# Kernel optimization log

Measured on AMD Instinct MI355X. Metric: run time of the kernel, lower is better.

The kernel has to match this reference:

```python
import jax, jax.numpy as jnp
import numpy as np


def setup_inputs() -> dict:
    key = jax.random.key(0)
    ks = jax.random.split(key, 7)
    B, Q, K, H, D, R = 2, 2048, 2048, 16, 64, 32
    queries = jax.random.normal(ks[0], (B, Q, H, D), dtype=jnp.float32)
    keys = jax.random.normal(ks[1], (B, K, H, D), dtype=jnp.float32)
    values = jax.random.normal(ks[2], (B, K, H, D), dtype=jnp.float32)
    att_mask = jax.random.randint(ks[3], (B, Q, K), 0, 2, dtype=jnp.int32)
    relative_att_ids = jax.random.randint(ks[4], (B, Q, K), 0, R, dtype=jnp.int32)
    # TruncatedNormal(stddev=0.5) approximated by clipped normal
    relative_emb_table = jnp.clip(
        0.5 * jax.random.normal(ks[5], (R, H, D), dtype=jnp.float32), -1.0, 1.0)
    relative_bias_table = jnp.zeros((R, H), dtype=jnp.float32)
    return {
        'queries': queries,
        'keys': keys,
        'values': values,
        'att_mask': att_mask,
        'relative_att_ids': relative_att_ids,
        'relative_emb_table': relative_emb_table,
        'relative_bias_table': relative_bias_table,
    }


def reference(queries, keys, values, att_mask, relative_att_ids,
              relative_emb_table, relative_bias_table):
    # content scores: [B,Q,K,H]
    content = jnp.einsum('bqhd,bkhd->bqkh', queries, keys)
    # relative scores per vocab id: [B,Q,R,H]
    all_rel = jnp.einsum('bqhd,rhd->bqrh', queries, relative_emb_table)
    all_rel = all_rel + relative_bias_table  # broadcast [R,H]
    # gather along vocab axis per (q,k): [B,Q,K,H]
    rel = jnp.take_along_axis(
        all_rel, relative_att_ids[:, :, :, None].astype(jnp.int32), axis=2)
    scores = content + rel
    d = queries.shape[-1]
    scores = scores / jnp.sqrt(jnp.asarray(d, scores.dtype))
    mask_adder = -10000.0 * (1.0 - att_mask[:, :, :, None].astype(scores.dtype))
    scores = scores + mask_adder
    probs = jax.nn.softmax(scores, axis=-2)  # softmax over key axis
    return jnp.einsum('bqkh,bkhd->bqhd', probs, values)
```

## Files before the change

kernel.cpp:

```cpp
#include <hip/hip_runtime.h>
#include <hip/hip_fp16.h>
#include <stdint.h>

#define Bn 2
#define Qn 2048
#define Kn 2048
#define Hn 16
#define Dn 64
#define Rn 32

#define LOG2E_8 0.18033688011112042f
#define MASK_NEG -14426.950408889634f

typedef __attribute__((ext_vector_type(8))) short short8v;
typedef __attribute__((ext_vector_type(4))) float f32x4;
typedef __attribute__((ext_vector_type(4))) uint32_t u32x4;

static __device__ __forceinline__ uint16_t bf16rn(float f) {
  uint32_t u = __builtin_bit_cast(uint32_t, f);
  u += 0x7FFFu + ((u >> 16) & 1u);
  return (uint16_t)(u >> 16);
}
static __device__ __forceinline__ float bf16f(uint16_t h) {
  uint32_t u = ((uint32_t)h) << 16;
  return __builtin_bit_cast(float, u);
}
static __device__ __forceinline__ float exp2a(float x) {
  float r; asm("v_exp_f32 %0, %1" : "=v"(r) : "v"(x)); return r;
}
static __device__ __forceinline__ uint32_t cvtpk(float lo, float hi) {
  uint32_t r; asm("v_cvt_pk_bf16_f32 %0, %1, %2" : "=v"(r) : "v"(lo), "v"(hi)); return r;
}
static __device__ __forceinline__ void gl_lds16(const void* g, void* l) {
  __builtin_amdgcn_global_load_lds((const __attribute__((address_space(1))) void*)g,
                                   (__attribute__((address_space(3))) void*)l, 16, 0, 0);
}

__global__ void pack_kernel(const int* __restrict__ ids,
                            const int* __restrict__ msk,
                            uint32_t* __restrict__ outp, int n4) {
  int i = blockIdx.x * 256 + threadIdx.x;
  if (i >= n4) return;
  int4 a = reinterpret_cast<const int4*>(ids)[i];
  int4 m = reinterpret_cast<const int4*>(msk)[i];
  uint32_t v = (uint32_t)((a.x | (m.x << 5)) & 0x3f)
             | ((uint32_t)((a.y | (m.y << 5)) & 0x3f) << 8)
             | ((uint32_t)((a.z | (m.z << 5)) & 0x3f) << 16)
             | ((uint32_t)((a.w | (m.w << 5)) & 0x3f) << 24);
  outp[i] = v;
}

__global__ __launch_bounds__(256) void kfrag6_kernel(const float* __restrict__ Kg,
                                                     const float* __restrict__ Vg,
                                                     uint8_t* __restrict__ frag) {
  const int bid = blockIdx.x;
  const int c = bid & 63;
  const int h = (bid >> 6) & 15;
  const int b = bid >> 10;
  uint8_t* panel = frag + (size_t)(b * 16 + h) * 524288u + (size_t)c * 8192u;
  uint4* kf = reinterpret_cast<uint4*>(panel);
  uint4* vf = reinterpret_cast<uint4*>(panel + 4096);
  const int tid = threadIdx.x;
  const int sdq = tid & 7, srow = (tid >> 3) & 15, stile = tid >> 7;
  const int sg = sdq & 3, sdm = sdq >> 2;
  const float* kp = Kg + ((((size_t)b * Kn) + c * 32 + stile * 16 + srow) * Hn + h) * Dn + (sdm * 32 + sg * 4);
  const float4 x0 = *reinterpret_cast<const float4*>(kp);
  const float4 x1 = *reinterpret_cast<const float4*>(kp + 16);
  const float xs0[4] = {x0.x * LOG2E_8, x0.y * LOG2E_8, x0.z * LOG2E_8, x0.w * LOG2E_8};
  const float xs1[4] = {x1.x * LOG2E_8, x1.y * LOG2E_8, x1.z * LOG2E_8, x1.w * LOG2E_8};
  uint4 uh;
  uh.x = bf16rn(xs0[0]) | ((uint32_t)bf16rn(xs0[1]) << 16);
  uh.y = bf16rn(xs0[2]) | ((uint32_t)bf16rn(xs0[3]) << 16);
  uh.z = bf16rn(xs1[0]) | ((uint32_t)bf16rn(xs1[1]) << 16);
  uh.w = bf16rn(xs1[2]) | ((uint32_t)bf16rn(xs1[3]) << 16);
  kf[(stile * 2 + sdm) * 64 + (srow + 16 * sg)] = uh;
  const int vd = tid & 63, vkq = tid >> 6;
  const float* vp = Vg + ((((size_t)b * Kn) + c * 32 + vkq * 4) * Hn + h) * Dn + vd;
  float v0[4], v1[4];
#pragma unroll
  for (int i = 0; i < 4; ++i) {
    v0[i] = vp[i * (Hn * Dn)];
    v1[i] = vp[(16 + i) * (Hn * Dn)];
  }
  uint4 uv;
  uv.x = bf16rn(v0[0]) | ((uint32_t)bf16rn(v0[1]) << 16);
  uv.y = bf16rn(v0[2]) | ((uint32_t)bf16rn(v0[3]) << 16);
  uv.z = bf16rn(v1[0]) | ((uint32_t)bf16rn(v1[1]) << 16);
  uv.w = bf16rn(v1[2]) | ((uint32_t)bf16rn(v1[3]) << 16);
  vf[(vd >> 4) * 64 + (vd & 15) + 16 * vkq] = uv;
}

__global__ __launch_bounds__(256, 2) void attn7_kernel(
    const float* __restrict__ Qg, const float* __restrict__ Eg,
    const float* __restrict__ biasg, const uint8_t* __restrict__ packed,
    const uint8_t* __restrict__ kfragp, float* __restrict__ outg) {
  __shared__ alignas(16) char smem[75520];
  __half* const tab   = reinterpret_cast<__half*>(smem);
  char* const cb0 = smem + 16896;
  char* const cb1 = smem + 33280;
  float* const q_lds  = reinterpret_cast<float*>(smem + 49664);
  float* const et_lds = reinterpret_cast<float*>(smem + 67072);

  const int tid = threadIdx.x;
  const int lane = tid & 63;
  const int w = tid >> 6;
  const int qr = lane & 15;
  const int g = lane >> 4;

  const int wi = (blockIdx.x & 7) * 64 + (blockIdx.x >> 3);
  const int qt = wi & 15;
  const int h = (wi >> 4) & 15;
  const int b = wi >> 8;
  const int q0 = qt * 128;

  const uint8_t* sbase = kfragp + (size_t)(b * 16 + h) * 524288u +
                         (size_t)w * 4096 + (size_t)lane * 16;
  {
    char* ld = cb0 + w * 4096;
    gl_lds16(sbase, ld);
    gl_lds16(sbase + 1024, ld + 1024);
    gl_lds16(sbase + 2048, ld + 2048);
    gl_lds16(sbase + 3072, ld + 3072);
  }

  short8v qhi[2][2];

#pragma unroll
  for (int half = 0; half < 2; ++half) {
    {
      const int row = tid >> 2, dq = (tid & 3) * 16;
      const float4* s4 = reinterpret_cast<const float4*>(
          Qg + (((size_t)b * Qn + q0 + half * 64 + row) * Hn + h) * Dn + dq);
      float4* dst = reinterpret_cast<float4*>(&q_lds[row * 68 + dq]);
#pragma unroll
      for (int i = 0; i < 4; ++i) dst[i] = s4[i];
    }
    if (half == 0) {
      const int r = tid >> 3, d0 = (tid & 7) * 8;
      const float* src = Eg + ((r * Hn + h) * Dn + d0);
#pragma unroll
      for (int i = 0; i < 8; ++i) et_lds[(d0 + i) * 33 + r] = src[i];
    }
    __syncthreads();
#pragma unroll
    for (int t = 0; t < 2; ++t) {
      const int ql = w * 32 + t * 16 + qr;
      if ((ql >> 6) == half) {
        const int rl = ql & 63;
#pragma unroll
        for (int dm = 0; dm < 2; ++dm) {
#pragma unroll
          for (int j = 0; j < 8; ++j) {
            const int dl = (j < 4) ? (4 * g + j) : (16 + 4 * g + (j - 4));
            qhi[t][dm][j] = (short)bf16rn(q_lds[rl * 68 + dm * 32 + dl]);
          }
        }
      }
    }
    {
      const int r = tid & 31, q8 = tid >> 5;
      float a8[8] = {0.f, 0.f, 0.f, 0.f, 0.f, 0.f, 0.f, 0.f};
      const float bias = biasg[r * Hn + h];
      for (int d = 0; d < 64; ++d) {
        const float e = et_lds[d * 33 + r];
#pragma unroll
        for (int i = 0; i < 8; ++i) a8[i] += e * q_lds[(q8 * 8 + i) * 68 + d];
      }
#pragma unroll
      for (int i = 0; i < 8; ++i) {
        const float ar = LOG2E_8 * (a8[i] + bias);
        const int qq = half * 64 + q8 * 8 + i;
        tab[qq * 66 + r]      = __float2half(ar + MASK_NEG);
        tab[qq * 66 + 32 + r] = __float2half(ar);
      }
    }
    __syncthreads();
  }

  int64_t prow[2];
  int trow[2];
#pragma unroll
  for (int t = 0; t < 2; ++t) {
    prow[t] = ((int64_t)(b * Qn + q0 + w * 32 + t * 16 + qr)) * Kn + 4 * g;
    trow[t] = (w * 32 + t * 16 + qr) * 66;
  }

  uint32_t pc[2][4], pn[2][4] = {{0u,0u,0u,0u},{0u,0u,0u,0u}};
#pragma unroll
  for (int t = 0; t < 2; ++t)
#pragma unroll
    for (int j = 0; j < 4; ++j)
      pc[t][j] = *reinterpret_cast<const uint32_t*>(packed + prow[t] + j * 16);

  char* cbc = cb0;
  char* cbn = cb1;
  asm volatile("s_waitcnt vmcnt(0)" ::: "memory");
  __builtin_amdgcn_sched_barrier(0);
  __syncthreads();

  const short8v ones = {(short)0x3F80, (short)0x3F80, (short)0x3F80, (short)0x3F80,
                        (short)0x3F80, (short)0x3F80, (short)0x3F80, (short)0x3F80};

  f32x4 acc[2][4] = {{{0.f,0.f,0.f,0.f},{0.f,0.f,0.f,0.f},{0.f,0.f,0.f,0.f},{0.f,0.f,0.f,0.f}},
                     {{0.f,0.f,0.f,0.f},{0.f,0.f,0.f,0.f},{0.f,0.f,0.f,0.f},{0.f,0.f,0.f,0.f}}};
  f32x4 accl[2] = {{0.f,0.f,0.f,0.f},{0.f,0.f,0.f,0.f}};

  for (int c = 0; c < 32; ++c) {
    if (c + 1 < 32) {
      const uint8_t* gs = sbase + (size_t)(c + 1) * 16384u;
      char* ld = cbn + w * 4096;
      gl_lds16(gs, ld); gl_lds16(gs + 1024, ld + 1024);
      gl_lds16(gs + 2048, ld + 2048); gl_lds16(gs + 3072, ld + 3072);
      const int64_t kb = (int64_t)(c + 1) * 64;
#pragma unroll
      for (int t = 0; t < 2; ++t)
#pragma unroll
        for (int j = 0; j < 4; ++j)
          pn[t][j] = *reinterpret_cast<const uint32_t*>(packed + prow[t] + kb + j * 16);
    }

    const short8v* kfs = reinterpret_cast<const short8v*>(cbc);
    f32x4 s[2][4] = {{{0.f,0.f,0.f,0.f},{0.f,0.f,0.f,0.f},{0.f,0.f,0.f,0.f},{0.f,0.f,0.f,0.f}},
                     {{0.f,0.f,0.f,0.f},{0.f,0.f,0.f,0.f},{0.f,0.f,0.f,0.f},{0.f,0.f,0.f,0.f}}};
    __builtin_amdgcn_s_setprio(1);
#pragma unroll
    for (int sub = 0; sub < 2; ++sub) {
      const int sb = sub * 512;
#pragma unroll
      for (int dm = 0; dm < 2; ++dm) {
        const short8v k0 = kfs[sb + dm * 64 + lane];
        const short8v k1 = kfs[sb + (2 + dm) * 64 + lane];
#pragma unroll
        for (int t = 0; t < 2; ++t) {
          s[t][sub * 2 + 0] =
              __builtin_amdgcn_mfma_f32_16x16x32_bf16(k0, qhi[t][dm], s[t][sub * 2 + 0], 0, 0, 0);
          s[t][sub * 2 + 1] =
              __builtin_amdgcn_mfma_f32_16x16x32_bf16(k1, qhi[t][dm], s[t][sub * 2 + 1], 0, 0, 0);
        }
      }
    }
    __builtin_amdgcn_s_setprio(0);

    short8v vv[2][4];
#pragma unroll
    for (int sub = 0; sub < 2; ++sub) {
      const short8v* vb = reinterpret_cast<const short8v*>(cbc + sub * 8192 + 4096);
#pragma unroll
      for (int dt = 0; dt < 4; ++dt) vv[sub][dt] = vb[dt * 64 + lane];
    }

#pragma unroll
    for (int t = 0; t < 2; ++t) {
      float pv[16];
#pragma unroll
      for (int i = 0; i < 16; ++i) {
        const int j = i >> 2, r = i & 3;
        const uint32_t v = (pc[t][j] >> (8 * r)) & 63u;
        pv[i] = exp2a(s[t][j][r] + __half2float(tab[trow[t] + (int)v]));
      }
      u32x4 pu0, pu1;
      pu0[0] = cvtpk(pv[0], pv[1]);   pu0[1] = cvtpk(pv[2], pv[3]);
      pu0[2] = cvtpk(pv[4], pv[5]);   pu0[3] = cvtpk(pv[6], pv[7]);
      pu1[0] = cvtpk(pv[8], pv[9]);   pu1[1] = cvtpk(pv[10], pv[11]);
      pu1[2] = cvtpk(pv[12], pv[13]); pu1[3] = cvtpk(pv[14], pv[15]);
      const short8v pa0 = __builtin_bit_cast(short8v, pu0);
      const short8v pa1 = __builtin_bit_cast(short8v, pu1);
      __builtin_amdgcn_s_setprio(1);
#pragma unroll
      for (int dt = 0; dt < 4; ++dt) {
        acc[t][dt] = __builtin_amdgcn_mfma_f32_16x16x32_bf16(pa0, vv[0][dt], acc[t][dt], 0, 0, 0);
        acc[t][dt] = __builtin_amdgcn_mfma_f32_16x16x32_bf16(pa1, vv[1][dt], acc[t][dt], 0, 0, 0);
      }
      accl[t] = __builtin_amdgcn_mfma_f32_16x16x32_bf16(pa0, ones, accl[t], 0, 0, 0);
      accl[t] = __builtin_amdgcn_mfma_f32_16x16x32_bf16(pa1, ones, accl[t], 0, 0, 0);
      __builtin_amdgcn_s_setprio(0);
    }

#pragma unroll
    for (int t = 0; t < 2; ++t)
#pragma unroll
      for (int j = 0; j < 4; ++j) pc[t][j] = pn[t][j];

    asm volatile("s_waitcnt vmcnt(0)" ::: "memory");
    __builtin_amdgcn_sched_barrier(0);
    __syncthreads();
    char* tmp = cbc; cbc = cbn; cbn = tmp;
  }

#pragma unroll
  for (int t = 0; t < 2; ++t) {
    f32x4 linv;
#pragma unroll
    for (int r = 0; r < 4; ++r) linv[r] = 1.0f / fmaxf(accl[t][r], 1e-35f);
#pragma unroll
    for (int dt = 0; dt < 4; ++dt)
#pragma unroll
      for (int r = 0; r < 4; ++r) {
        const int qrow = q0 + w * 32 + t * 16 + 4 * g + r;
        outg[(((size_t)b * Qn + qrow) * Hn + h) * Dn + dt * 16 + qr] = acc[t][dt][r] * linv[r];
      }
  }
}

__global__ __launch_bounds__(256) void attn_old_kernel(
    const float* __restrict__ Qg, const float* __restrict__ Kg,
    const float* __restrict__ Vg, const int* __restrict__ maskg,
    const int* __restrict__ idsg, const float* __restrict__ Eg,
    const float* __restrict__ biasg, float* __restrict__ outg) {
  __shared__ alignas(16) char smem[34304];
  float* const allrel = reinterpret_cast<float*>(smem);
  float* const q_lds  = reinterpret_cast<float*>(smem + 8448);
  float* const et_lds = reinterpret_cast<float*>(smem + 25856);
  uint4* const kfrag  = reinterpret_cast<uint4*>(smem + 8448);
  uint4* const vfrag  = reinterpret_cast<uint4*>(smem + 16640);

  const int tid  = threadIdx.x;
  const int lane = tid & 63;
  const int w    = tid >> 6;
  const int qr   = lane & 15;
  const int g    = lane >> 4;

  const int bid = blockIdx.x;
  const int h  = bid & 15;
  const int qt = (bid >> 4) & 31;
  const int b  = bid >> 9;
  const int q0 = qt * 64;

  {
    const int row = tid >> 2, dq = (tid & 3) * 16;
    const float4* s4 =
        reinterpret_cast<const float4*>(Qg + (((b * Qn) + q0 + row) * Hn + h) * Dn + dq);
    float4* dst = reinterpret_cast<float4*>(&q_lds[row * 68 + dq]);
#pragma unroll
    for (int i = 0; i < 4; ++i) dst[i] = s4[i];
  }
  {
    const int r = tid >> 3, d0 = (tid & 7) * 8;
    const float* src = Eg + ((r * Hn + h) * Dn + d0);
#pragma unroll
    for (int i = 0; i < 8; ++i) et_lds[(d0 + i) * 33 + r] = src[i];
  }
  __syncthreads();

  const int qloc = w * 16 + qr;
  short8v qhi[2], qlo[2];
#pragma unroll
  for (int dm = 0; dm < 2; ++dm) {
#pragma unroll
    for (int j = 0; j < 8; ++j) {
      const int dl = (j < 4) ? (4 * g + j) : (16 + 4 * g + (j - 4));
      const float x = q_lds[qloc * 68 + dm * 32 + dl];
      const uint16_t hi = bf16rn(x);
      qhi[dm][j] = (short)hi;
      qlo[dm][j] = (short)bf16rn(x - bf16f(hi));
    }
  }

  {
    const int r = tid & 31, q8 = tid >> 5;
    float acc[8] = {0.f, 0.f, 0.f, 0.f, 0.f, 0.f, 0.f, 0.f};
    const float bias = biasg[r * Hn + h];
    for (int d = 0; d < 64; ++d) {
      const float e = et_lds[d * 33 + r];
#pragma unroll
      for (int i = 0; i < 8; ++i) acc[i] += e * q_lds[(q8 * 8 + i) * 68 + d];
    }
#pragma unroll
    for (int i = 0; i < 8; ++i)
      allrel[(q8 * 8 + i) * 33 + r] = 0.125f * (acc[i] + bias);
  }
  __syncthreads();

  const int sdq = tid & 7, srow = (tid >> 3) & 15, stile = tid >> 7;
  const int sg = sdq & 3, sdm = sdq >> 2;
  int koff = (((b * Kn) + stile * 16 + srow) * Hn + h) * Dn + (sdm * 32 + sg * 4);
  const int kslotH = (stile * 2 + sdm) * 64 + (srow + 16 * sg);
  const int kslotL = (4 + stile * 2 + sdm) * 64 + (srow + 16 * sg);
  const int vd = tid & 63, vkq = tid >> 6;
  int voff = (((b * Kn) + vkq * 4) * Hn + h) * Dn + vd;
  const int vslot = (vd >> 4) * 64 + (vd & 15) + 16 * vkq;

  const int qglob = q0 + qloc;
  const int prow = (b * Qn + qglob) * Kn + 4 * g;

  f32x4 acc[4] = {{0.f,0.f,0.f,0.f},{0.f,0.f,0.f,0.f},{0.f,0.f,0.f,0.f},{0.f,0.f,0.f,0.f}};
  float mrun = -1e30f, lrun = 0.f;

  const short8v* kfs = reinterpret_cast<const short8v*>(kfrag);
  const short8v* vfs = reinterpret_cast<const short8v*>(vfrag);

  for (int c = 0; c < 64; ++c) {
    const int kb = c * 32;
    __syncthreads();
    {
      const float4 x0 = *reinterpret_cast<const float4*>(Kg + koff);
      const float4 x1 = *reinterpret_cast<const float4*>(Kg + koff + 16);
      koff += 32 * Hn * Dn;
      const float xs0[4] = {x0.x, x0.y, x0.z, x0.w};
      const float xs1[4] = {x1.x, x1.y, x1.z, x1.w};
      uint16_t hh[8], ll[8];
#pragma unroll
      for (int i = 0; i < 4; ++i) {
        const uint16_t h0 = bf16rn(xs0[i]);
        const uint16_t h1 = bf16rn(xs1[i]);
        hh[i] = h0; hh[4 + i] = h1;
        ll[i] = bf16rn(xs0[i] - bf16f(h0));
        ll[4 + i] = bf16rn(xs1[i] - bf16f(h1));
      }
      uint4 uh, ul;
      uh.x = hh[0] | ((uint32_t)hh[1] << 16); uh.y = hh[2] | ((uint32_t)hh[3] << 16);
      uh.z = hh[4] | ((uint32_t)hh[5] << 16); uh.w = hh[6] | ((uint32_t)hh[7] << 16);
      ul.x = ll[0] | ((uint32_t)ll[1] << 16); ul.y = ll[2] | ((uint32_t)ll[3] << 16);
      ul.z = ll[4] | ((uint32_t)ll[5] << 16); ul.w = ll[6] | ((uint32_t)ll[7] << 16);
      kfrag[kslotH] = uh;
      kfrag[kslotL] = ul;
    }
    {
      float v0[4], v1[4];
#pragma unroll
      for (int i = 0; i < 4; ++i) {
        v0[i] = Vg[voff + i * (Hn * Dn)];
        v1[i] = Vg[voff + 16 * Hn * Dn + i * (Hn * Dn)];
      }
      voff += 32 * Hn * Dn;
      uint4 uv;
      uv.x = bf16rn(v0[0]) | ((uint32_t)bf16rn(v0[1]) << 16);
      uv.y = bf16rn(v0[2]) | ((uint32_t)bf16rn(v0[3]) << 16);
      uv.z = bf16rn(v1[0]) | ((uint32_t)bf16rn(v1[1]) << 16);
      uv.w = bf16rn(v1[2]) | ((uint32_t)bf16rn(v1[3]) << 16);
      vfrag[vslot] = uv;
    }
    __syncthreads();

    f32x4 s0 = {0.f, 0.f, 0.f, 0.f}, s1 = {0.f, 0.f, 0.f, 0.f};
#pragma unroll
    for (int dm = 0; dm < 2; ++dm) {
      const short8v k0h = kfs[(dm) * 64 + lane];
      const short8v k1h = kfs[(2 + dm) * 64 + lane];
      const short8v k0l = kfs[(4 + dm) * 64 + lane];
      const short8v k1l = kfs[(6 + dm) * 64 + lane];
      s0 = __builtin_amdgcn_mfma_f32_16x16x32_bf16(k0h, qhi[dm], s0, 0, 0, 0);
      s1 = __builtin_amdgcn_mfma_f32_16x16x32_bf16(k1h, qhi[dm], s1, 0, 0, 0);
      s0 = __builtin_amdgcn_mfma_f32_16x16x32_bf16(k0h, qlo[dm], s0, 0, 0, 0);
      s1 = __builtin_amdgcn_mfma_f32_16x16x32_bf16(k1h, qlo[dm], s1, 0, 0, 0);
      s0 = __builtin_amdgcn_mfma_f32_16x16x32_bf16(k0l, qhi[dm], s0, 0, 0, 0);
      s1 = __builtin_amdgcn_mfma_f32_16x16x32_bf16(k1l, qhi[dm], s1, 0, 0, 0);
    }

    float sv[8];
    {
      const int ib = prow + kb;
      const int4 i0 = *reinterpret_cast<const int4*>(idsg + ib);
      const int4 i1 = *reinterpret_cast<const int4*>(idsg + ib + 16);
      const int4 m0 = *reinterpret_cast<const int4*>(maskg + ib);
      const int4 m1 = *reinterpret_cast<const int4*>(maskg + ib + 16);
      const int ia0[4] = {i0.x, i0.y, i0.z, i0.w};
      const int ia1[4] = {i1.x, i1.y, i1.z, i1.w};
      const int ma0[4] = {m0.x, m0.y, m0.z, m0.w};
      const int ma1[4] = {m1.x, m1.y, m1.z, m1.w};
#pragma unroll
      for (int r = 0; r < 4; ++r) {
        sv[r]     = 0.125f * s0[r] + allrel[qloc * 33 + ia0[r]] + (ma0[r] ? 0.f : -10000.f);
        sv[4 + r] = 0.125f * s1[r] + allrel[qloc * 33 + ia1[r]] + (ma1[r] ? 0.f : -10000.f);
      }
    }

    float m8 = sv[0];
#pragma unroll
    for (int i = 1; i < 8; ++i) m8 = fmaxf(m8, sv[i]);
    m8 = fmaxf(m8, __shfl_xor(m8, 16));
    m8 = fmaxf(m8, __shfl_xor(m8, 32));
    const float mnew = fmaxf(mrun, m8);
    const float sc = __expf(mrun - mnew);
    mrun = mnew;
    float pv[8];
    float ps = 0.f;
#pragma unroll
    for (int i = 0; i < 8; ++i) { pv[i] = __expf(sv[i] - mnew); ps += pv[i]; }
    ps += __shfl_xor(ps, 16);
    ps += __shfl_xor(ps, 32);
    lrun = lrun * sc + ps;

    f32x4 scv;
#pragma unroll
    for (int r = 0; r < 4; ++r) scv[r] = __shfl(sc, 4 * g + r);
#pragma unroll
    for (int dt = 0; dt < 4; ++dt) acc[dt] *= scv;

    short8v pa;
#pragma unroll
    for (int i = 0; i < 8; ++i) pa[i] = (short)bf16rn(pv[i]);
#pragma unroll
    for (int dt = 0; dt < 4; ++dt)
      acc[dt] = __builtin_amdgcn_mfma_f32_16x16x32_bf16(pa, vfs[dt * 64 + lane], acc[dt], 0, 0, 0);
  }

  const float linv = 1.0f / lrun;
  f32x4 lv;
#pragma unroll
  for (int r = 0; r < 4; ++r) lv[r] = __shfl(linv, 4 * g + r);
#pragma unroll
  for (int dt = 0; dt < 4; ++dt) {
#pragma unroll
    for (int r = 0; r < 4; ++r) {
      const int qrow = q0 + w * 16 + 4 * g + r;
      outg[(((b * Qn) + qrow) * Hn + h) * Dn + dt * 16 + qr] = acc[dt][r] * lv[r];
    }
  }
}

extern "C" void kernel_launch(void* const* d_in, const int* in_sizes, int n_in,
                              void* d_out, int out_size, void* d_ws, size_t ws_size,
                              hipStream_t stream) {
  const float* Qg    = (const float*)d_in[0];
  const float* Kg    = (const float*)d_in[1];
  const float* Vg    = (const float*)d_in[2];
  const int*   maskg = (const int*)d_in[3];
  const int*   idsg  = (const int*)d_in[4];
  const float* Eg    = (const float*)d_in[5];
  const float* biasg = (const float*)d_in[6];
  float* outg = (float*)d_out;

  const size_t oPack = 0;
  const size_t oK    = 8388608;
  const size_t need6 = 25165824;
  const int n4 = (Bn * Qn * Kn) / 4;

  uint8_t* ws = (uint8_t*)d_ws;

  if (ws_size >= need6) {
    pack_kernel<<<n4 / 256, 256, 0, stream>>>(idsg, maskg, (uint32_t*)(ws + oPack), n4);
    kfrag6_kernel<<<Bn * Hn * 64, 256, 0, stream>>>(Kg, Vg, ws + oK);
    attn7_kernel<<<Bn * Hn * (Qn / 128), 256, 0, stream>>>(
        Qg, Eg, biasg, ws + oPack, ws + oK, outg);
  } else {
    attn_old_kernel<<<Bn * Hn * (Qn / 64), 256, 0, stream>>>(
        Qg, Kg, Vg, maskg, idsg, Eg, biasg, outg);
  }
}
```

Measured before the change: 107.6 us.

## Split key range across two wave groups and precompute relative table in separate kernel

```diff
diff --git a/kernel.cpp b/kernel.cpp
--- a/kernel.cpp
+++ b/kernel.cpp
@@ -20,10 +20,6 @@
   uint32_t u = __builtin_bit_cast(uint32_t, f);
   u += 0x7FFFu + ((u >> 16) & 1u);
   return (uint16_t)(u >> 16);
-}
-static __device__ __forceinline__ float bf16f(uint16_t h) {
-  uint32_t u = ((uint32_t)h) << 16;
-  return __builtin_bit_cast(float, u);
 }
 static __device__ __forceinline__ float exp2a(float x) {
   float r; asm("v_exp_f32 %0, %1" : "=v"(r) : "v"(x)); return r;
@@ -90,20 +86,63 @@
   vf[(vd >> 4) * 64 + (vd & 15) + 16 * vkq] = uv;
 }
 
-__global__ __launch_bounds__(256, 2) void attn7_kernel(
-    const float* __restrict__ Qg, const float* __restrict__ Eg,
-    const float* __restrict__ biasg, const uint8_t* __restrict__ packed,
-    const uint8_t* __restrict__ kfragp, float* __restrict__ outg) {
-  __shared__ alignas(16) char smem[75520];
-  __half* const tab   = reinterpret_cast<__half*>(smem);
-  char* const cb0 = smem + 16896;
-  char* const cb1 = smem + 33280;
-  float* const q_lds  = reinterpret_cast<float*>(smem + 49664);
-  float* const et_lds = reinterpret_cast<float*>(smem + 67072);
-
+__global__ __launch_bounds__(256) void tab_kernel(const float* __restrict__ Qg,
+                                                  const float* __restrict__ Eg,
+                                                  const float* __restrict__ biasg,
+                                                  __half* __restrict__ tabg) {
+  __shared__ alignas(16) char smem[25856];
+  float* const q_lds = reinterpret_cast<float*>(smem);
+  float* const et    = reinterpret_cast<float*>(smem + 17408);
+  const int tid = threadIdx.x;
+  const int bid = blockIdx.x;
+  const int qt = bid & 31;
+  const int h  = (bid >> 5) & 15;
+  const int b  = bid >> 9;
+  const int q0 = qt * 64;
+  {
+    const int row = tid >> 2, dq = (tid & 3) * 16;
+    const float4* s4 = reinterpret_cast<const float4*>(
+        Qg + (((size_t)b * Qn + q0 + row) * Hn + h) * Dn + dq);
+    float4* dst = reinterpret_cast<float4*>(&q_lds[row * 68 + dq]);
+#pragma unroll
+    for (int i = 0; i < 4; ++i) dst[i] = s4[i];
+  }
+  {
+    const int r = tid >> 3, d0 = (tid & 7) * 8;
+    const float* src = Eg + ((r * Hn + h) * Dn + d0);
+#pragma unroll
+    for (int i = 0; i < 8; ++i) et[(d0 + i) * 33 + r] = src[i];
+  }
+  __syncthreads();
+  {
+    const int r = tid & 31, q8 = tid >> 5;
+    float a8[8] = {0.f, 0.f, 0.f, 0.f, 0.f, 0.f, 0.f, 0.f};
+    const float bias = biasg[r * Hn + h];
+    for (int d = 0; d < 64; ++d) {
+      const float e = et[d * 33 + r];
+#pragma unroll
+      for (int i = 0; i < 8; ++i) a8[i] += e * q_lds[(q8 * 8 + i) * 68 + d];
+    }
+#pragma unroll
+    for (int i = 0; i < 8; ++i) {
+      const float ar = LOG2E_8 * (a8[i] + bias);
+      const size_t rowo = ((size_t)(b * 16 + h) * 2048 + q0 + q8 * 8 + i) * 64;
+      tabg[rowo + r]      = __float2half(ar + MASK_NEG);
+      tabg[rowo + 32 + r] = __float2half(ar);
+    }
+  }
+}
+
+__global__ __launch_bounds__(512, 4) void attn8_kernel(
+    const float* __restrict__ Qg, const uint8_t* __restrict__ packed,
+    const uint8_t* __restrict__ kfragp, const __half* __restrict__ tabg,
+    float* __restrict__ outg) {
+  __shared__ alignas(16) char smem[49152];
   const int tid = threadIdx.x;
   const int lane = tid & 63;
   const int w = tid >> 6;
+  const int w4 = w & 3;
+  const int ks = w >> 2;
   const int qr = lane & 15;
   const int g = lane >> 4;
 
@@ -113,192 +152,162 @@
   const int b = wi >> 8;
   const int q0 = qt * 128;
 
+  char* const myhalf = smem + 16384 + ks * 16384;
+
+  {
+    const uint8_t* tsrc = reinterpret_cast<const uint8_t*>(
+        tabg + ((size_t)(b * 16 + h) * 2048 + q0) * 64);
+    char* ld = smem + w * 2048;
+    gl_lds16(tsrc + (size_t)w * 2048 + (size_t)lane * 16, ld);
+    gl_lds16(tsrc + (size_t)w * 2048 + 1024 + (size_t)lane * 16, ld + 1024);
+  }
   const uint8_t* sbase = kfragp + (size_t)(b * 16 + h) * 524288u +
-                         (size_t)w * 4096 + (size_t)lane * 16;
-  {
-    char* ld = cb0 + w * 4096;
+                         (size_t)(ks * 32) * 8192u + (size_t)w4 * 2048 + (size_t)lane * 16;
+  {
+    char* ld = myhalf + w4 * 2048;
     gl_lds16(sbase, ld);
     gl_lds16(sbase + 1024, ld + 1024);
-    gl_lds16(sbase + 2048, ld + 2048);
-    gl_lds16(sbase + 3072, ld + 3072);
   }
 
   short8v qhi[2][2];
-
-#pragma unroll
-  for (int half = 0; half < 2; ++half) {
-    {
-      const int row = tid >> 2, dq = (tid & 3) * 16;
-      const float4* s4 = reinterpret_cast<const float4*>(
-          Qg + (((size_t)b * Qn + q0 + half * 64 + row) * Hn + h) * Dn + dq);
-      float4* dst = reinterpret_cast<float4*>(&q_lds[row * 68 + dq]);
-#pragma unroll
-      for (int i = 0; i < 4; ++i) dst[i] = s4[i];
-    }
-    if (half == 0) {
-      const int r = tid >> 3, d0 = (tid & 7) * 8;
-      const float* src = Eg + ((r * Hn + h) * Dn + d0);
-#pragma unroll
-      for (int i = 0; i < 8; ++i) et_lds[(d0 + i) * 33 + r] = src[i];
-    }
-    __syncthreads();
-#pragma unroll
-    for (int t = 0; t < 2; ++t) {
-      const int ql = w * 32 + t * 16 + qr;
-      if ((ql >> 6) == half) {
-        const int rl = ql & 63;
-#pragma unroll
-        for (int dm = 0; dm < 2; ++dm) {
-#pragma unroll
-          for (int j = 0; j < 8; ++j) {
-            const int dl = (j < 4) ? (4 * g + j) : (16 + 4 * g + (j - 4));
-            qhi[t][dm][j] = (short)bf16rn(q_lds[rl * 68 + dm * 32 + dl]);
-          }
-        }
-      }
-    }
-    {
-      const int r = tid & 31, q8 = tid >> 5;
-      float a8[8] = {0.f, 0.f, 0.f, 0.f, 0.f, 0.f, 0.f, 0.f};
-      const float bias = biasg[r * Hn + h];
-      for (int d = 0; d < 64; ++d) {
-        const float e = et_lds[d * 33 + r];
-#pragma unroll
-        for (int i = 0; i < 8; ++i) a8[i] += e * q_lds[(q8 * 8 + i) * 68 + d];
-      }
-#pragma unroll
-      for (int i = 0; i < 8; ++i) {
-        const float ar = LOG2E_8 * (a8[i] + bias);
-        const int qq = half * 64 + q8 * 8 + i;
-        tab[qq * 66 + r]      = __float2half(ar + MASK_NEG);
-        tab[qq * 66 + 32 + r] = __float2half(ar);
-      }
-    }
-    __syncthreads();
-  }
+#pragma unroll
+  for (int t = 0; t < 2; ++t)
+#pragma unroll
+    for (int dm = 0; dm < 2; ++dm) {
+      const float* qp = Qg + (((size_t)b * Qn + q0 + w4 * 32 + t * 16 + qr) * Hn + h) * Dn +
+                        dm * 32 + 4 * g;
+      const float4 x0 = *reinterpret_cast<const float4*>(qp);
+      const float4 x1 = *reinterpret_cast<const float4*>(qp + 16);
+      u32x4 u;
+      u[0] = cvtpk(x0.x, x0.y); u[1] = cvtpk(x0.z, x0.w);
+      u[2] = cvtpk(x1.x, x1.y); u[3] = cvtpk(x1.z, x1.w);
+      qhi[t][dm] = __builtin_bit_cast(short8v, u);
+    }
 
   int64_t prow[2];
   int trow[2];
 #pragma unroll
   for (int t = 0; t < 2; ++t) {
-    prow[t] = ((int64_t)(b * Qn + q0 + w * 32 + t * 16 + qr)) * Kn + 4 * g;
-    trow[t] = (w * 32 + t * 16 + qr) * 66;
-  }
-
-  uint32_t pc[2][4], pn[2][4] = {{0u,0u,0u,0u},{0u,0u,0u,0u}};
+    prow[t] = ((int64_t)(b * Qn + q0 + w4 * 32 + t * 16 + qr)) * Kn + ks * 1024 + 4 * g;
+    trow[t] = (w4 * 32 + t * 16 + qr) * 64;
+  }
+  uint32_t pc[2][2], pn[2][2] = {{0u, 0u}, {0u, 0u}};
 #pragma unroll
   for (int t = 0; t < 2; ++t)
 #pragma unroll
-    for (int j = 0; j < 4; ++j)
-      pc[t][j] = *reinterpret_cast<const uint32_t*>(packed + prow[t] + j * 16);
-
-  char* cbc = cb0;
-  char* cbn = cb1;
+    for (int st = 0; st < 2; ++st)
+      pc[t][st] = *reinterpret_cast<const uint32_t*>(packed + prow[t] + st * 16);
+
   asm volatile("s_waitcnt vmcnt(0)" ::: "memory");
   __builtin_amdgcn_sched_barrier(0);
   __syncthreads();
 
   const short8v ones = {(short)0x3F80, (short)0x3F80, (short)0x3F80, (short)0x3F80,
                         (short)0x3F80, (short)0x3F80, (short)0x3F80, (short)0x3F80};
+  const __half* tabh = reinterpret_cast<const __half*>(smem);
 
   f32x4 acc[2][4] = {{{0.f,0.f,0.f,0.f},{0.f,0.f,0.f,0.f},{0.f,0.f,0.f,0.f},{0.f,0.f,0.f,0.f}},
                      {{0.f,0.f,0.f,0.f},{0.f,0.f,0.f,0.f},{0.f,0.f,0.f,0.f},{0.f,0.f,0.f,0.f}}};
   f32x4 accl[2] = {{0.f,0.f,0.f,0.f},{0.f,0.f,0.f,0.f}};
+  int cbuf = 0;
 
   for (int c = 0; c < 32; ++c) {
     if (c + 1 < 32) {
-      const uint8_t* gs = sbase + (size_t)(c + 1) * 16384u;
-      char* ld = cbn + w * 4096;
-      gl_lds16(gs, ld); gl_lds16(gs + 1024, ld + 1024);
-      gl_lds16(gs + 2048, ld + 2048); gl_lds16(gs + 3072, ld + 3072);
-      const int64_t kb = (int64_t)(c + 1) * 64;
+      const uint8_t* gs = sbase + (size_t)(c + 1) * 8192u;
+      char* ld = myhalf + (cbuf ^ 1) * 8192 + w4 * 2048;
+      gl_lds16(gs, ld);
+      gl_lds16(gs + 1024, ld + 1024);
+      const int64_t kb = (int64_t)(c + 1) * 32;
 #pragma unroll
       for (int t = 0; t < 2; ++t)
 #pragma unroll
-        for (int j = 0; j < 4; ++j)
-          pn[t][j] = *reinterpret_cast<const uint32_t*>(packed + prow[t] + kb + j * 16);
-    }
-
-    const short8v* kfs = reinterpret_cast<const short8v*>(cbc);
-    f32x4 s[2][4] = {{{0.f,0.f,0.f,0.f},{0.f,0.f,0.f,0.f},{0.f,0.f,0.f,0.f},{0.f,0.f,0.f,0.f}},
-                     {{0.f,0.f,0.f,0.f},{0.f,0.f,0.f,0.f},{0.f,0.f,0.f,0.f},{0.f,0.f,0.f,0.f}}};
+        for (int st = 0; st < 2; ++st)
+          pn[t][st] = *reinterpret_cast<const uint32_t*>(packed + prow[t] + kb + st * 16);
+    }
+
+    const short8v* kfs = reinterpret_cast<const short8v*>(myhalf + cbuf * 8192);
+    f32x4 s[2][2] = {{{0.f,0.f,0.f,0.f},{0.f,0.f,0.f,0.f}},
+                     {{0.f,0.f,0.f,0.f},{0.f,0.f,0.f,0.f}}};
     __builtin_amdgcn_s_setprio(1);
 #pragma unroll
-    for (int sub = 0; sub < 2; ++sub) {
-      const int sb = sub * 512;
-#pragma unroll
-      for (int dm = 0; dm < 2; ++dm) {
-        const short8v k0 = kfs[sb + dm * 64 + lane];
-        const short8v k1 = kfs[sb + (2 + dm) * 64 + lane];
-#pragma unroll
-        for (int t = 0; t < 2; ++t) {
-          s[t][sub * 2 + 0] =
-              __builtin_amdgcn_mfma_f32_16x16x32_bf16(k0, qhi[t][dm], s[t][sub * 2 + 0], 0, 0, 0);
-          s[t][sub * 2 + 1] =
-              __builtin_amdgcn_mfma_f32_16x16x32_bf16(k1, qhi[t][dm], s[t][sub * 2 + 1], 0, 0, 0);
-        }
+    for (int dm = 0; dm < 2; ++dm) {
+      const short8v k0 = kfs[dm * 64 + lane];
+      const short8v k1 = kfs[(2 + dm) * 64 + lane];
+#pragma unroll
+      for (int t = 0; t < 2; ++t) {
+        s[t][0] = __builtin_amdgcn_mfma_f32_16x16x32_bf16(k0, qhi[t][dm], s[t][0], 0, 0, 0);
+        s[t][1] = __builtin_amdgcn_mfma_f32_16x16x32_bf16(k1, qhi[t][dm], s[t][1], 0, 0, 0);
       }
     }
     __builtin_amdgcn_s_setprio(0);
 
-    short8v vv[2][4];
-#pragma unroll
-    for (int sub = 0; sub < 2; ++sub) {
-      const short8v* vb = reinterpret_cast<const short8v*>(cbc + sub * 8192 + 4096);
-#pragma unroll
-      for (int dt = 0; dt < 4; ++dt) vv[sub][dt] = vb[dt * 64 + lane];
-    }
+    const short8v* vfs = reinterpret_cast<const short8v*>(myhalf + cbuf * 8192 + 4096);
+    short8v vv[4];
+#pragma unroll
+    for (int dt = 0; dt < 4; ++dt) vv[dt] = vfs[dt * 64 + lane];
 
 #pragma unroll
     for (int t = 0; t < 2; ++t) {
-      float pv[16];
-#pragma unroll
-      for (int i = 0; i < 16; ++i) {
-        const int j = i >> 2, r = i & 3;
-        const uint32_t v = (pc[t][j] >> (8 * r)) & 63u;
-        pv[i] = exp2a(s[t][j][r] + __half2float(tab[trow[t] + (int)v]));
+      float pv[8];
+#pragma unroll
+      for (int i = 0; i < 8; ++i) {
+        const int st = i >> 2, r = i & 3;
+        const uint32_t v = (pc[t][st] >> (8 * r)) & 63u;
+        pv[i] = exp2a(s[t][st][r] + __half2float(tabh[trow[t] + (int)v]));
       }
-      u32x4 pu0, pu1;
-      pu0[0] = cvtpk(pv[0], pv[1]);   pu0[1] = cvtpk(pv[2], pv[3]);
-      pu0[2] = cvtpk(pv[4], pv[5]);   pu0[3] = cvtpk(pv[6], pv[7]);
-      pu1[0] = cvtpk(pv[8], pv[9]);   pu1[1] = cvtpk(pv[10], pv[11]);
-      pu1[2] = cvtpk(pv[12], pv[13]); pu1[3] = cvtpk(pv[14], pv[15]);
-      const short8v pa0 = __builtin_bit_cast(short8v, pu0);
-      const short8v pa1 = __builtin_bit_cast(short8v, pu1);
+      u32x4 pu;
+      pu[0] = cvtpk(pv[0], pv[1]); pu[1] = cvtpk(pv[2], pv[3]);
+      pu[2] = cvtpk(pv[4], pv[5]); pu[3] = cvtpk(pv[6], pv[7]);
+      const short8v pa = __builtin_bit_cast(short8v, pu);
       __builtin_amdgcn_s_setprio(1);
 #pragma unroll
-      for (int dt = 0; dt < 4; ++dt) {
-        acc[t][dt] = __builtin_amdgcn_mfma_f32_16x16x32_bf16(pa0, vv[0][dt], acc[t][dt], 0, 0, 0);
-        acc[t][dt] = __builtin_amdgcn_mfma_f32_16x16x32_bf16(pa1, vv[1][dt], acc[t][dt], 0, 0, 0);
-      }
-      accl[t] = __builtin_amdgcn_mfma_f32_16x16x32_bf16(pa0, ones, accl[t], 0, 0, 0);
-      accl[t] = __builtin_amdgcn_mfma_f32_16x16x32_bf16(pa1, ones, accl[t], 0, 0, 0);
+      for (int dt = 0; dt < 4; ++dt)
+        acc[t][dt] = __builtin_amdgcn_mfma_f32_16x16x32_bf16(pa, vv[dt], acc[t][dt], 0, 0, 0);
+      accl[t] = __builtin_amdgcn_mfma_f32_16x16x32_bf16(pa, ones, accl[t], 0, 0, 0);
       __builtin_amdgcn_s_setprio(0);
     }
 
 #pragma unroll
-    for (int t = 0; t < 2; ++t)
-#pragma unroll
-      for (int j = 0; j < 4; ++j) pc[t][j] = pn[t][j];
+    for (int t = 0; t < 2; ++t) { pc[t][0] = pn[t][0]; pc[t][1] = pn[t][1]; }
 
     asm volatile("s_waitcnt vmcnt(0)" ::: "memory");
     __builtin_amdgcn_sched_barrier(0);
     __syncthreads();
-    char* tmp = cbc; cbc = cbn; cbn = tmp;
-  }
-
-#pragma unroll
-  for (int t = 0; t < 2; ++t) {
-    f32x4 linv;
-#pragma unroll
-    for (int r = 0; r < 4; ++r) linv[r] = 1.0f / fmaxf(accl[t][r], 1e-35f);
-#pragma unroll
-    for (int dt = 0; dt < 4; ++dt)
-#pragma unroll
-      for (int r = 0; r < 4; ++r) {
-        const int qrow = q0 + w * 32 + t * 16 + 4 * g + r;
-        outg[(((size_t)b * Qn + qrow) * Hn + h) * Dn + dt * 16 + qr] = acc[t][dt][r] * linv[r];
-      }
+    cbuf ^= 1;
+  }
+
+  float* const acc1s = reinterpret_cast<float*>(smem + 16384);
+  float* const l1s   = reinterpret_cast<float*>(smem);
+  if (ks == 1) {
+#pragma unroll
+    for (int t = 0; t < 2; ++t) {
+#pragma unroll
+      for (int dt = 0; dt < 4; ++dt)
+#pragma unroll
+        for (int r = 0; r < 4; ++r)
+          acc1s[(w4 * 32 + t * 16 + 4 * g + r) * 64 + dt * 16 + qr] = acc[t][dt][r];
+#pragma unroll
+      for (int r = 0; r < 4; ++r)
+        l1s[w4 * 32 + t * 16 + 4 * g + r] = accl[t][r];
+    }
+  }
+  __syncthreads();
+  if (ks == 0) {
+#pragma unroll
+    for (int t = 0; t < 2; ++t) {
+      const f32x4 l1v = *reinterpret_cast<const f32x4*>(&l1s[w4 * 32 + t * 16 + 4 * g]);
+      f32x4 linv;
+#pragma unroll
+      for (int r = 0; r < 4; ++r) linv[r] = 1.0f / (accl[t][r] + l1v[r]);
+#pragma unroll
+      for (int dt = 0; dt < 4; ++dt)
+#pragma unroll
+        for (int r = 0; r < 4; ++r) {
+          const int lrow = w4 * 32 + t * 16 + 4 * g + r;
+          const float o = (acc[t][dt][r] + acc1s[lrow * 64 + dt * 16 + qr]) * linv[r];
+          outg[(((size_t)b * Qn + q0 + lrow) * Hn + h) * Dn + dt * 16 + qr] = o;
+        }
+    }
   }
 }
 
@@ -352,7 +361,8 @@
       const float x = q_lds[qloc * 68 + dm * 32 + dl];
       const uint16_t hi = bf16rn(x);
       qhi[dm][j] = (short)hi;
-      qlo[dm][j] = (short)bf16rn(x - bf16f(hi));
+      const float lo = x - __builtin_bit_cast(float, (uint32_t)hi << 16);
+      qlo[dm][j] = (short)bf16rn(lo);
     }
   }
 
@@ -404,8 +414,8 @@
         const uint16_t h0 = bf16rn(xs0[i]);
         const uint16_t h1 = bf16rn(xs1[i]);
         hh[i] = h0; hh[4 + i] = h1;
-        ll[i] = bf16rn(xs0[i] - bf16f(h0));
-        ll[4 + i] = bf16rn(xs1[i] - bf16f(h1));
+        ll[i] = bf16rn(xs0[i] - __builtin_bit_cast(float, (uint32_t)h0 << 16));
+        ll[4 + i] = bf16rn(xs1[i] - __builtin_bit_cast(float, (uint32_t)h1 << 16));
       }
       uint4 uh, ul;
       uh.x = hh[0] | ((uint32_t)hh[1] << 16); uh.y = hh[2] | ((uint32_t)hh[3] << 16);
@@ -523,16 +533,18 @@
 
   const size_t oPack = 0;
   const size_t oK    = 8388608;
-  const size_t need6 = 25165824;
+  const size_t oT    = 25165824;
+  const size_t need8 = 33554432;
   const int n4 = (Bn * Qn * Kn) / 4;
 
   uint8_t* ws = (uint8_t*)d_ws;
 
-  if (ws_size >= need6) {
+  if (ws_size >= need8) {
     pack_kernel<<<n4 / 256, 256, 0, stream>>>(idsg, maskg, (uint32_t*)(ws + oPack), n4);
     kfrag6_kernel<<<Bn * Hn * 64, 256, 0, stream>>>(Kg, Vg, ws + oK);
-    attn7_kernel<<<Bn * Hn * (Qn / 128), 256, 0, stream>>>(
-        Qg, Eg, biasg, ws + oPack, ws + oK, outg);
+    tab_kernel<<<Bn * Hn * 32, 256, 0, stream>>>(Qg, Eg, biasg, (__half*)(ws + oT));
+    attn8_kernel<<<Bn * Hn * (Qn / 128), 512, 0, stream>>>(
+        Qg, ws + oPack, ws + oK, (const __half*)(ws + oT), outg);
   } else {
     attn_old_kernel<<<Bn * Hn * (Qn / 64), 256, 0, stream>>>(
         Qg, Kg, Vg, maskg, idsg, Eg, biasg, outg);
```

After: 114.3 us. 1.06x slower.
